# Kernel tuning notes

Measured on AMD Instinct MI355X. Metric: run time of the kernel, lower is better.

Reference implementation:

```python
import jax, jax.numpy as jnp
import numpy as np

DIM = 768
HEADS = 12
DHEAD = 64
N = 197  # 1 cls token + 14*14 patches
P = 196
KMAX = 9  # max neighborhood size (interior patch: 3x3 window)
SCALE = DHEAD ** -0.5


def _build_neighbors():
    """Reproduce the module's hard-coded kv_list; pad to KMAX with a mask."""
    top = set(range(2, 14))
    down = set(range(184, 196))
    left = set(range(15, 170, 14))
    right = set(range(28, 183, 14))
    idx = np.zeros((P, KMAX), np.int32)
    msk = np.zeros((P, KMAX), np.float32)
    for i in range(1, 197):
        if i == 1:
            nb = [1, 2, 15, 16]
        elif i == 14:
            nb = [13, 14, 27, 28]
        elif i == 183:
            nb = [169, 170, 183, 184]
        elif i == 196:
            nb = [181, 182, 195, 196]
        elif i in top:
            nb = [i - 1, i, i + 1, i + 13, i + 14, i + 15]
        elif i in left:
            nb = [i - 14, i - 13, i, i + 1, i + 14, i + 15]
        elif i in right:
            nb = [i - 15, i - 14, i - 1, i, i + 13, i + 14]
        elif i in down:
            nb = [i - 15, i - 14, i - 13, i - 1, i, i + 1]
        else:
            nb = [i - 15, i - 14, i - 13, i - 1, i, i + 1, i + 13, i + 14, i + 15]
        L = len(nb)
        idx[i - 1, :L] = nb
        msk[i - 1, :L] = 1.0
    return jnp.asarray(idx), jnp.asarray(msk)

NBR_IDX, NBR_MASK = _build_neighbors()


def setup_inputs() -> dict:
    key = jax.random.key(0)
    ks = jax.random.split(key, 10)
    b = 128
    w = lambda k: jax.random.normal(k, (DIM, DIM), jnp.float32) * 0.02
    bia = lambda k: jax.random.normal(k, (DIM,), jnp.float32) * 0.02
    return {
        "x_qkv": jax.random.normal(ks[0], (b, N, DIM), jnp.float32),
        "y_q": jax.random.normal(ks[1], (b, N, DIM), jnp.float32),
        "Wq": w(ks[2]), "bq": bia(ks[3]),
        "Wk": w(ks[4]), "bk": bia(ks[5]),
        "Wv": w(ks[6]), "bv": bia(ks[7]),
        "Wo": w(ks[8]), "bo": bia(ks[9]),
    }


def reference(x_qkv, y_q, Wq, bq, Wk, bk, Wv, bv, Wo, bo):
    b = x_qkv.shape[0]
    split = lambda t: t.reshape(b, N, HEADS, DHEAD).transpose(0, 2, 1, 3)  # b h n d
    k = split(x_qkv @ Wk + bk)
    v = split(x_qkv @ Wv + bv)
    q = split(y_q @ Wq + bq)

    # token 0 (cls): full attention over all N keys
    dots0 = jnp.einsum('bhd,bhjd->bhj', q[:, :, 0], k) * SCALE
    out0 = jnp.einsum('bhj,bhjd->bhd', jax.nn.softmax(dots0, axis=-1), v)[:, :, None]  # b h 1 d

    # patches 1..196: gather local windows (padded to KMAX, masked)
    kn = k[:, :, NBR_IDX]  # b h P KMAX d
    vn = v[:, :, NBR_IDX]
    dots = jnp.einsum('bhpd,bhpjd->bhpj', q[:, :, 1:], kn) * SCALE
    big_neg = jnp.asarray(jnp.finfo(dots.dtype).min, dots.dtype)
    dots = jnp.where(NBR_MASK > 0, dots, big_neg)
    attn = jax.nn.softmax(dots, axis=-1)
    outp = jnp.einsum('bhpj,bhpjd->bhpd', attn, vn)  # b h P d

    out = jnp.concatenate([out0, outp], axis=2)           # b h N d
    out = out.transpose(0, 2, 1, 3).reshape(b, N, HEADS * DHEAD)
    return out @ Wo + bo  # dropout: eval mode (identity)
```

## Files before the change

kernel.cpp:

```cpp
#include <hip/hip_runtime.h>


typedef __bf16 bf16x8 __attribute__((ext_vector_type(8)));
typedef float f32x4 __attribute__((ext_vector_type(4)));

#define NTOK 197
#define BATCH 128
#define MROWS (BATCH * NTOK)
#define MTILES_FULL (MROWS / 128)
#define NB_FULL (6 * MTILES_FULL)
#define W_ELEMS ((size_t)768 * 768)
#define BUF_ELEMS_FULL ((size_t)MROWS * 768)
#define PATCH_NBLK (BATCH * 49 * 12 / 4)

#define CHUNK_B 8
#define NCHUNK 16
#define MC_CHUNK (CHUNK_B * NTOK)
#define MTILES_CHUNK 13
#define BUF_ELEMS_CHUNK ((size_t)MC_CHUNK * 768)

__device__ __forceinline__ unsigned short f2b(float f) {
  unsigned int x = __float_as_uint(f);
  x += 0x7fff + ((x >> 16) & 1);
  return (unsigned short)(x >> 16);
}

__device__ __forceinline__ uint4 cvt8pack(float4 f0, float4 f1) {
  unsigned short t8[8] = { f2b(f0.x), f2b(f0.y), f2b(f0.z), f2b(f0.w),
                           f2b(f1.x), f2b(f1.y), f2b(f1.z), f2b(f1.w) };
  return *(const uint4*)t8;
}

#define GLOAD_LDS16(gp, lp)                                                   \
  __builtin_amdgcn_global_load_lds(                                           \
      (const __attribute__((address_space(1))) void*)(gp),                    \
      (__attribute__((address_space(3))) void*)(lp), 16, 0, 0)

__device__ __forceinline__ int xcd_swizzle(int bid, int nb) {
  const int q = nb >> 3, r = nb & 7;
  const int xcd = bid & 7, i = bid >> 3;
  return (xcd < r ? xcd * (q + 1) : r * (q + 1) + (xcd - r) * q) + i;
}

__global__ void transpose768x4(const float* __restrict__ s0, const float* __restrict__ s1,
                               const float* __restrict__ s2, const float* __restrict__ s3,
                               unsigned short* __restrict__ d0, unsigned short* __restrict__ d1,
                               unsigned short* __restrict__ d2, unsigned short* __restrict__ d3) {
  const float* src;
  unsigned short* dst;
  switch (blockIdx.y) {
    case 0: src = s0; dst = d0; break;
    case 1: src = s1; dst = d1; break;
    case 2: src = s2; dst = d2; break;
    default: src = s3; dst = d3; break;
  }
  int idx = blockIdx.x * 256 + threadIdx.x;
  int n = idx / 768, k = idx % 768;
  dst[idx] = f2b(src[k * 768 + n]);
}

__global__ void cvt8(const float* __restrict__ src, unsigned short* __restrict__ dst,
                     const int n8) {
  int i = blockIdx.x * 256 + threadIdx.x;
  if (i >= n8) return;
  const float4* p = (const float4*)(src + (size_t)i * 8);
  *(uint4*)(dst + (size_t)i * 8) = cvt8pack(p[0], p[1]);
}

__device__ __forceinline__ void mfma_tile(const unsigned short* sA, const unsigned short* sB,
                                          f32x4 (&acc)[4][4],
                                          const int wr, const int wc,
                                          const int lane16, const int quad) {
  bf16x8 af[4], bf_[4];
  #pragma unroll
  for (int i = 0; i < 4; ++i)
    af[i] = *(const bf16x8*)&sA[(wr * 64 + i * 16 + lane16) * 32 + quad * 8];
  #pragma unroll
  for (int j = 0; j < 4; ++j)
    bf_[j] = *(const bf16x8*)&sB[(wc * 64 + j * 16 + lane16) * 32 + quad * 8];
  #pragma unroll
  for (int i = 0; i < 4; ++i)
    #pragma unroll
    for (int j = 0; j < 4; ++j)
      acc[i][j] = __builtin_amdgcn_mfma_f32_16x16x32_bf16(af[i], bf_[j], acc[i][j], 0, 0, 0);
}

__device__ __forceinline__ void mfma_tile_kv(const unsigned short* sA,
                                             const unsigned short* sBk,
                                             const unsigned short* sBv,
                                             f32x4 (&aK)[4][4], f32x4 (&aV)[4][4],
                                             const int wr, const int wc,
                                             const int lane16, const int quad) {
  bf16x8 af[4], b1[4], b2[4];
  #pragma unroll
  for (int i = 0; i < 4; ++i)
    af[i] = *(const bf16x8*)&sA[(wr * 64 + i * 16 + lane16) * 32 + quad * 8];
  #pragma unroll
  for (int j = 0; j < 4; ++j) {
    b1[j] = *(const bf16x8*)&sBk[(wc * 64 + j * 16 + lane16) * 32 + quad * 8];
    b2[j] = *(const bf16x8*)&sBv[(wc * 64 + j * 16 + lane16) * 32 + quad * 8];
  }
  #pragma unroll
  for (int i = 0; i < 4; ++i)
    #pragma unroll
    for (int j = 0; j < 4; ++j) {
      aK[i][j] = __builtin_amdgcn_mfma_f32_16x16x32_bf16(af[i], b1[j], aK[i][j], 0, 0, 0);
      aV[i][j] = __builtin_amdgcn_mfma_f32_16x16x32_bf16(af[i], b2[j], aV[i][j], 0, 0, 0);
    }
}

__device__ __forceinline__ void epilogue128(f32x4 (&acc)[4][4], const float* __restrict__ bias,
                                            float* __restrict__ C, const int row0, const int n0,
                                            const int wr, const int wc,
                                            const int lane16, const int quad) {
  #pragma unroll
  for (int j = 0; j < 4; ++j) {
    const int col = n0 + wc * 64 + j * 16 + lane16;
    const float bv = bias[col];
    #pragma unroll
    for (int i = 0; i < 4; ++i) {
      const int r0 = row0 + wr * 64 + i * 16 + quad * 4;
      #pragma unroll
      for (int r = 0; r < 4; ++r)
        C[(size_t)(r0 + r) * 768 + col] = acc[i][j][r] + bv;
    }
  }
}

__global__ __launch_bounds__(256, 2) void kv_gemm(
    const unsigned short* __restrict__ Xb,
    const unsigned short* __restrict__ WkT, const unsigned short* __restrict__ WvT,
    const float* __restrict__ bk, const float* __restrict__ bv,
    float* __restrict__ K, float* __restrict__ V) {
  __shared__ unsigned short lds[2][3][4096];
  const int swz = xcd_swizzle(blockIdx.x, NB_FULL);
  const int by = swz / 6, bx = swz % 6;
  const int row0 = by * 128, n0 = bx * 128;
  const int tid = threadIdx.x;
  const int l = tid & 63, w = tid >> 6;
  const int wr = w >> 1, wc = w & 1;
  const int lane16 = l & 15, quad = l >> 4;
  const int rr = tid >> 2, c8 = (tid & 3) * 8;
  const int wbase = (tid & 192) * 8;

  const unsigned short* a0 = Xb + (size_t)(row0 + rr) * 768 + c8;
  const unsigned short* a1 = a0 + (size_t)64 * 768;
  const unsigned short* k0p = WkT + (size_t)(n0 + rr) * 768 + c8;
  const unsigned short* k1p = k0p + (size_t)64 * 768;
  const unsigned short* v0p = WvT + (size_t)(n0 + rr) * 768 + c8;
  const unsigned short* v1p = v0p + (size_t)64 * 768;

  f32x4 aK[4][4] = {}, aV[4][4] = {};

#define STAGE_KV(B, kt) do { const int ko = (kt) * 32;            \
    GLOAD_LDS16(a0 + ko, &lds[B][0][wbase]);                      \
    GLOAD_LDS16(a1 + ko, &lds[B][0][wbase + 2048]);               \
    GLOAD_LDS16(k0p + ko, &lds[B][1][wbase]);                     \
    GLOAD_LDS16(k1p + ko, &lds[B][1][wbase + 2048]);              \
    GLOAD_LDS16(v0p + ko, &lds[B][2][wbase]);                     \
    GLOAD_LDS16(v1p + ko, &lds[B][2][wbase + 2048]); } while (0)

  STAGE_KV(0, 0);
  __syncthreads();
  for (int kt = 0; kt < 23; ++kt) {
    const int cur = kt & 1;
    STAGE_KV(cur ^ 1, kt + 1);
    mfma_tile_kv(&lds[cur][0][0], &lds[cur][1][0], &lds[cur][2][0],
                 aK, aV, wr, wc, lane16, quad);
    __syncthreads();
  }
  mfma_tile_kv(&lds[1][0][0], &lds[1][1][0], &lds[1][2][0],
               aK, aV, wr, wc, lane16, quad);
#undef STAGE_KV

  epilogue128(aK, bk, K, row0, n0, wr, wc, lane16, quad);
  epilogue128(aV, bv, V, row0, n0, wr, wc, lane16, quad);
}

__global__ __launch_bounds__(256, 2) void o_gemm(
    const unsigned short* __restrict__ Ab, const unsigned short* __restrict__ WoT,
    const float* __restrict__ bo, float* __restrict__ C) {
  __shared__ unsigned short lds[2][2][4096];
  const int swz = xcd_swizzle(blockIdx.x, NB_FULL);
  const int by = swz / 6, bx = swz % 6;
  const int row0 = by * 128, n0 = bx * 128;
  const int tid = threadIdx.x;
  const int l = tid & 63, w = tid >> 6;
  const int wr = w >> 1, wc = w & 1;
  const int lane16 = l & 15, quad = l >> 4;
  const int rr = tid >> 2, c8 = (tid & 3) * 8;
  const int wbase = (tid & 192) * 8;

  const unsigned short* a0 = Ab + (size_t)(row0 + rr) * 768 + c8;
  const unsigned short* a1 = a0 + (size_t)64 * 768;
  const unsigned short* b0 = WoT + (size_t)(n0 + rr) * 768 + c8;
  const unsigned short* b1 = b0 + (size_t)64 * 768;

  f32x4 acc[4][4] = {};

#define STAGE_O(B, kt) do { const int ko = (kt) * 32;             \
    GLOAD_LDS16(a0 + ko, &lds[B][0][wbase]);                      \
    GLOAD_LDS16(a1 + ko, &lds[B][0][wbase + 2048]);               \
    GLOAD_LDS16(b0 + ko, &lds[B][1][wbase]);                      \
    GLOAD_LDS16(b1 + ko, &lds[B][1][wbase + 2048]); } while (0)

  STAGE_O(0, 0);
  __syncthreads();
  for (int kt = 0; kt < 23; ++kt) {
    const int cur = kt & 1;
    STAGE_O(cur ^ 1, kt + 1);
    mfma_tile(&lds[cur][0][0], &lds[cur][1][0], acc, wr, wc, lane16, quad);
    __syncthreads();
  }
  mfma_tile(&lds[1][0][0], &lds[1][1][0], acc, wr, wc, lane16, quad);
#undef STAGE_O

  epilogue128(acc, bo, C, row0, n0, wr, wc, lane16, quad);
}

__global__ __launch_bounds__(256, 2) void q_gemm(
    const float* __restrict__ Y, const unsigned short* __restrict__ WqT,
    const float* __restrict__ bq, float* __restrict__ Q) {
  __shared__ unsigned short As[2][4096];
  __shared__ unsigned short Bs[2][4096];
  const int swz = xcd_swizzle(blockIdx.x, NB_FULL);
  const int by = swz / 6, bx = swz % 6;
  const int row0 = by * 128, n0 = bx * 128;
  const int tid = threadIdx.x;
  const int l = tid & 63, w = tid >> 6;
  const int wr = w >> 1, wc = w & 1;
  const int lane16 = l & 15, quad = l >> 4;
  const int rr = tid >> 2, c8 = (tid & 3) * 8;
  const int wbase = (tid & 192) * 8;

  const float* y0 = Y + (size_t)(row0 + rr) * 768 + c8;
  const float* y1 = y0 + (size_t)64 * 768;
  const unsigned short* b0 = WqT + (size_t)(n0 + rr) * 768 + c8;
  const unsigned short* b1 = b0 + (size_t)64 * 768;

  f32x4 acc[4][4] = {};

  float4 f0 = *(const float4*)y0, f1 = *(const float4*)(y0 + 4);
  float4 g0 = *(const float4*)y1, g1 = *(const float4*)(y1 + 4);
  GLOAD_LDS16(b0, &Bs[0][wbase]);
  GLOAD_LDS16(b1, &Bs[0][wbase + 2048]);
  *(uint4*)&As[0][rr * 32 + c8] = cvt8pack(f0, f1);
  *(uint4*)&As[0][(64 + rr) * 32 + c8] = cvt8pack(g0, g1);
  __syncthreads();

  for (int kt = 0; kt < 23; ++kt) {
    const int cur = kt & 1, nxt = cur ^ 1;
    const int ko = (kt + 1) * 32;
    f0 = *(const float4*)(y0 + ko); f1 = *(const float4*)(y0 + ko + 4);
    g0 = *(const float4*)(y1 + ko); g1 = *(const float4*)(y1 + ko + 4);
    GLOAD_LDS16(b0 + ko, &Bs[nxt][wbase]);
    GLOAD_LDS16(b1 + ko, &Bs[nxt][wbase + 2048]);
    mfma_tile(&As[cur][0], &Bs[cur][0], acc, wr, wc, lane16, quad);
    *(uint4*)&As[nxt][rr * 32 + c8] = cvt8pack(f0, f1);
    *(uint4*)&As[nxt][(64 + rr) * 32 + c8] = cvt8pack(g0, g1);
    __syncthreads();
  }
  mfma_tile(&As[1][0], &Bs[1][0], acc, wr, wc, lane16, quad);

  epilogue128(acc, bq, Q, row0, n0, wr, wc, lane16, quad);
}

__device__ __forceinline__ void gemm_body_f32A(
    const float* __restrict__ A, const unsigned short* __restrict__ Wt,
    const float* __restrict__ bias, float* __restrict__ C,
    const int row0, const int n0, const int Mrows, unsigned short* sAB) {
  const int tid = threadIdx.x;
  const int l = tid & 63, w = tid >> 6;
  const int wr = w >> 1, wc = w & 1;
  const int lane16 = l & 15, quad = l >> 4;

  f32x4 acc[4][4] = {};

  for (int kt = 0; kt < 24; ++kt) {
    const int k0 = kt * 32;
    #pragma unroll
    for (int i = 0; i < 2; ++i) {
      const int ch = i * 256 + tid;
      const int rr2 = ch >> 2;
      const int c82 = (ch & 3) * 8;
      int ra = row0 + rr2; if (ra > Mrows - 1) ra = Mrows - 1;
      const float* ap = A + (size_t)ra * 768 + k0 + c82;
      float4 q0 = *(const float4*)ap;
      float4 q1 = *(const float4*)(ap + 4);
      *(uint4*)&sAB[rr2 * 32 + c82] = cvt8pack(q0, q1);
      uint4 vb = *(const uint4*)(Wt + (size_t)(n0 + rr2) * 768 + k0 + c82);
      *(uint4*)&sAB[4096 + rr2 * 32 + c82] = vb;
    }
    __syncthreads();
    mfma_tile(sAB, sAB + 4096, acc, wr, wc, lane16, quad);
    __syncthreads();
  }
  #pragma unroll
  for (int j = 0; j < 4; ++j) {
    const int col = n0 + wc * 64 + j * 16 + lane16;
    const float bv = bias[col];
    #pragma unroll
    for (int i = 0; i < 4; ++i) {
      const int r0 = row0 + wr * 64 + i * 16 + quad * 4;
      #pragma unroll
      for (int r = 0; r < 4; ++r)
        if (r0 + r < Mrows)
          C[(size_t)(r0 + r) * 768 + col] = acc[i][j][r] + bv;
    }
  }
}

__global__ __launch_bounds__(256, 2) void qkv_gemm(
    const float* __restrict__ X, const float* __restrict__ Y,
    const unsigned short* __restrict__ WkT, const unsigned short* __restrict__ WvT,
    const unsigned short* __restrict__ WqT,
    const float* __restrict__ bk, const float* __restrict__ bv, const float* __restrict__ bq,
    float* __restrict__ K, float* __restrict__ V, float* __restrict__ Q,
    const int Mrows) {
  __shared__ unsigned short sAB[8192];
  const int mat = blockIdx.x / 6;
  const int n0 = (blockIdx.x % 6) * 128;
  const float* A = (mat == 2) ? Y : X;
  const unsigned short* Wt = (mat == 0) ? WkT : (mat == 1) ? WvT : WqT;
  const float* bias = (mat == 0) ? bk : (mat == 1) ? bv : bq;
  float* C = (mat == 0) ? K : (mat == 1) ? V : Q;
  gemm_body_f32A(A, Wt, bias, C, blockIdx.y * 128, n0, Mrows, sAB);
}

__global__ __launch_bounds__(256, 2) void gemm_bt(
    const float* __restrict__ A, const unsigned short* __restrict__ Wt,
    const float* __restrict__ bias, float* __restrict__ C, const int Mrows) {
  __shared__ unsigned short sAB[8192];
  gemm_body_f32A(A, Wt, bias, C, blockIdx.y * 128, blockIdx.x * 128, Mrows, sAB);
}

__device__ __forceinline__ float cls_attn_body(const float* __restrict__ Q,
                                               const float* __restrict__ K,
                                               const float* __restrict__ V,
                                               const size_t rowbase,
                                               float* q, float* attn, float* red) {
  const int tid = threadIdx.x, l = tid & 63, w = tid >> 6;
  if (tid < 64) q[tid] = Q[rowbase + tid];
  __syncthreads();

  float d = -3e38f;
  if (tid < NTOK) {
    const float4* Kp = (const float4*)(K + rowbase + (size_t)tid * 768);
    float s = 0.f;
    #pragma unroll
    for (int u = 0; u < 16; ++u) {
      float4 kk = Kp[u];
      s += q[u * 4 + 0] * kk.x + q[u * 4 + 1] * kk.y
         + q[u * 4 + 2] * kk.z + q[u * 4 + 3] * kk.w;
    }
    d = s * 0.125f;
  }
  float m = d;
  #pragma unroll
  for (int off = 32; off; off >>= 1) m = fmaxf(m, __shfl_xor(m, off, 64));
  if (l == 0) red[w] = m;
  __syncthreads();
  const float M = fmaxf(fmaxf(red[0], red[1]), fmaxf(red[2], red[3]));
  float e = (tid < NTOK) ? __expf(d - M) : 0.f;
  float ssum = e;
  #pragma unroll
  for (int off = 32; off; off >>= 1) ssum += __shfl_xor(ssum, off, 64);
  if (l == 0) red[4 + w] = ssum;
  __syncthreads();
  const float S = red[4] + red[5] + red[6] + red[7];
  attn[tid] = e / S;
  __syncthreads();
  float o = 0.f;
  if (tid < 64) {
    for (int j = 0; j < NTOK; ++j)
      o += attn[j] * V[rowbase + (size_t)j * 768 + tid];
  }
  return o;
}

__global__ void cls_attn_b(const float* __restrict__ Q, const float* __restrict__ K,
                           const float* __restrict__ V, unsigned short* __restrict__ ATT) {
  __shared__ float q[64];
  __shared__ float attn[256];
  __shared__ float red[8];
  const int b = blockIdx.x / 12, h = blockIdx.x % 12;
  const size_t rowbase = ((size_t)b * NTOK) * 768 + h * 64;
  float o = cls_attn_body(Q, K, V, rowbase, q, attn, red);
  if (threadIdx.x < 64) ATT[rowbase + threadIdx.x] = f2b(o);
}

__global__ void cls_attn(const float* __restrict__ Q, const float* __restrict__ K,
                         const float* __restrict__ V, float* __restrict__ ATT) {
  __shared__ float q[64];
  __shared__ float attn[256];
  __shared__ float red[8];
  const int b = blockIdx.x / 12, h = blockIdx.x % 12;
  const size_t rowbase = ((size_t)b * NTOK) * 768 + h * 64;
  float o = cls_attn_body(Q, K, V, rowbase, q, attn, red);
  if (threadIdx.x < 64) ATT[rowbase + threadIdx.x] = o;
}

__global__ __launch_bounds__(256) void patch_attn4_b(
    const float* __restrict__ Q, const float* __restrict__ K,
    const float* __restrict__ V, unsigned short* __restrict__ ATT) {
  const int swb = xcd_swizzle(blockIdx.x, PATCH_NBLK);
  const int wu = swb * 4 + (threadIdx.x >> 6);
  const int l = threadIdx.x & 63;
  const int t16 = l & 15, pg = l >> 4;
  const int h = wu % 12;
  const int t2 = wu / 12;
  const int pq = t2 % 49;
  const int b = t2 / 49;
  const int p = pq * 4 + pg;
  const int r = p / 14, c = p % 14;
  const size_t ib = ((size_t)b * NTOK) * 768 + h * 64 + t16 * 4;

  const float4 q = *(const float4*)(Q + ib + (size_t)(p + 1) * 768);

  float s[9];
  int tok[9];
  #pragma unroll
  for (int jj = 0; jj < 9; ++jj) {
    const int nr = r + jj / 3 - 1, nc = c + jj % 3 - 1;
    const bool ok = ((unsigned)nr < 14u) && ((unsigned)nc < 14u);
    tok[jj] = ok ? (1 + nr * 14 + nc) : (p + 1);
    const float4 kk = *(const float4*)(K + ib + (size_t)tok[jj] * 768);
    float d = q.x * kk.x + q.y * kk.y + q.z * kk.z + q.w * kk.w;
    d += __shfl_xor(d, 1);
    d += __shfl_xor(d, 2);
    d += __shfl_xor(d, 4);
    d += __shfl_xor(d, 8);
    s[jj] = ok ? d * 0.125f : -3e38f;
  }
  float m = s[0];
  #pragma unroll
  for (int jj = 1; jj < 9; ++jj) m = fmaxf(m, s[jj]);
  float sum = 0.f;
  #pragma unroll
  for (int jj = 0; jj < 9; ++jj) { s[jj] = __expf(s[jj] - m); sum += s[jj]; }
  const float inv = 1.f / sum;

  float4 o = {0.f, 0.f, 0.f, 0.f};
  #pragma unroll
  for (int jj = 0; jj < 9; ++jj) {
    const float4 vv = *(const float4*)(V + ib + (size_t)tok[jj] * 768);
    o.x += s[jj] * vv.x; o.y += s[jj] * vv.y;
    o.z += s[jj] * vv.z; o.w += s[jj] * vv.w;
  }
  o.x *= inv; o.y *= inv; o.z *= inv; o.w *= inv;
  unsigned short t4[4] = { f2b(o.x), f2b(o.y), f2b(o.z), f2b(o.w) };
  *(ushort2*)&ATT[ib + (size_t)(p + 1) * 768] = *(const ushort2*)&t4[0];
  *(ushort2*)&ATT[ib + (size_t)(p + 1) * 768 + 2] = *(const ushort2*)&t4[2];
}

__device__ __forceinline__ float patch_attn_body(const float* __restrict__ Q,
                                                 const float* __restrict__ K,
                                                 const float* __restrict__ V,
                                                 const size_t base, const int p,
                                                 const int r, const int c) {
  const float qd = Q[base + (size_t)(p + 1) * 768];

  float s[9];
  int tok[9];
  #pragma unroll
  for (int jj = 0; jj < 9; ++jj) {
    const int nr = r + jj / 3 - 1, nc = c + jj % 3 - 1;
    const bool ok = ((unsigned)nr < 14u) && ((unsigned)nc < 14u);
    tok[jj] = ok ? (1 + nr * 14 + nc) : (p + 1);
    float d = qd * K[base + (size_t)tok[jj] * 768];
    #pragma unroll
    for (int off = 32; off; off >>= 1) d += __shfl_xor(d, off, 64);
    s[jj] = ok ? d * 0.125f : -3e38f;
  }
  float m = s[0];
  #pragma unroll
  for (int jj = 1; jj < 9; ++jj) m = fmaxf(m, s[jj]);
  float sum = 0.f;
  #pragma unroll
  for (int jj = 0; jj < 9; ++jj) { s[jj] = __expf(s[jj] - m); sum += s[jj]; }
  const float inv = 1.f / sum;
  float o = 0.f;
  #pragma unroll
  for (int jj = 0; jj < 9; ++jj) o += s[jj] * V[base + (size_t)tok[jj] * 768];
  return o * inv;
}

__global__ void patch_attn(const float* __restrict__ Q, const float* __restrict__ K,
                           const float* __restrict__ V, float* __restrict__ ATT) {
  const int wgid = blockIdx.x * 4 + (threadIdx.x >> 6);
  const int l = threadIdx.x & 63;
  const int h = wgid % 12;
  const int t2 = wgid / 12;
  const int p = t2 % 196;
  const int b = t2 / 196;
  const int r = p / 14, c = p % 14;
  const size_t base = ((size_t)b * NTOK) * 768 + h * 64 + l;
  float o = patch_attn_body(Q, K, V, base, p, r, c);
  ATT[base + (size_t)(p + 1) * 768] = o;
}

extern "C" void kernel_launch(void* const* d_in, const int* in_sizes, int n_in,
                              void* d_out, int out_size, void* d_ws, size_t ws_size,
                              hipStream_t stream) {
  const float* x  = (const float*)d_in[0];
  const float* y  = (const float*)d_in[1];
  const float* Wq = (const float*)d_in[2];
  const float* bq = (const float*)d_in[3];
  const float* Wk = (const float*)d_in[4];
  const float* bk = (const float*)d_in[5];
  const float* Wv = (const float*)d_in[6];
  const float* bv = (const float*)d_in[7];
  const float* Wo = (const float*)d_in[8];
  const float* bo = (const float*)d_in[9];
  float* out = (float*)d_out;

  unsigned short* WqT = (unsigned short*)d_ws;
  unsigned short* WkT = WqT + W_ELEMS;
  unsigned short* WvT = WkT + W_ELEMS;
  unsigned short* WoT = WvT + W_ELEMS;

  transpose768x4<<<dim3(2304, 4), 256, 0, stream>>>(Wq, Wk, Wv, Wo, WqT, WkT, WvT, WoT);

  const size_t need_full = 4 * W_ELEMS * sizeof(unsigned short)
                         + BUF_ELEMS_FULL * sizeof(unsigned short)
                         + 3 * BUF_ELEMS_FULL * sizeof(float);
  if (ws_size >= need_full) {
    unsigned short* Xb = WoT + W_ELEMS;
    unsigned short* ATTb = Xb;
    float* Kc = (float*)(Xb + BUF_ELEMS_FULL);
    float* Vc = Kc + BUF_ELEMS_FULL;
    float* Qc = Vc + BUF_ELEMS_FULL;

    const int n8 = (int)(BUF_ELEMS_FULL / 8);
    cvt8<<<n8 / 256, 256, 0, stream>>>(x, Xb, n8);

    kv_gemm<<<NB_FULL, 256, 0, stream>>>(Xb, WkT, WvT, bk, bv, Kc, Vc);
    q_gemm<<<NB_FULL, 256, 0, stream>>>(y, WqT, bq, Qc);
    cls_attn_b<<<BATCH * 12, 256, 0, stream>>>(Qc, Kc, Vc, ATTb);
    patch_attn4_b<<<PATCH_NBLK, 256, 0, stream>>>(Qc, Kc, Vc, ATTb);
    o_gemm<<<NB_FULL, 256, 0, stream>>>(ATTb, WoT, bo, out);
  } else {
    float* Kc = (float*)(WoT + W_ELEMS);
    float* Vc = Kc + BUF_ELEMS_CHUNK;
    float* Qc = Vc + BUF_ELEMS_CHUNK;

    for (int c = 0; c < NCHUNK; ++c) {
      const float* xc = x + (size_t)c * BUF_ELEMS_CHUNK;
      const float* yc = y + (size_t)c * BUF_ELEMS_CHUNK;
      qkv_gemm<<<dim3(18, MTILES_CHUNK), 256, 0, stream>>>(
          xc, yc, WkT, WvT, WqT, bk, bv, bq, Kc, Vc, Qc, MC_CHUNK);
      cls_attn<<<CHUNK_B * 12, 256, 0, stream>>>(Qc, Kc, Vc, Qc);
      patch_attn<<<(CHUNK_B * 196 * 12) / 4, 256, 0, stream>>>(Qc, Kc, Vc, Qc);
      gemm_bt<<<dim3(6, MTILES_CHUNK), 256, 0, stream>>>(Qc, WoT, bo,
                                                         out + (size_t)c * BUF_ELEMS_CHUNK, MC_CHUNK);
    }
  }
}
```

Baseline: 556.1 us.

## Unify projections into one bf16 GEMM with finer pipeline sync and parallel CLS reduction

Replaces the fused K/V GEMM and the fp32-input Q GEMM with a single bf16 GEMM kernel launched four times. Y is pre-converted to bf16 with cvt8 into the reused buffer. The GEMM loop swaps __syncthreads for explicit vmcnt waits plus raw barriers, and launch bounds rise to 4 blocks per CU to allow more occupancy. CLS attention now splits the V reduction across all four waves instead of one. The cost is reading X twice and an extra conversion pass over Y.

```diff
diff --git a/kernel.cpp b/kernel.cpp
--- a/kernel.cpp
+++ b/kernel.cpp
@@ -85,30 +85,6 @@
       acc[i][j] = __builtin_amdgcn_mfma_f32_16x16x32_bf16(af[i], bf_[j], acc[i][j], 0, 0, 0);
 }
 
-__device__ __forceinline__ void mfma_tile_kv(const unsigned short* sA,
-                                             const unsigned short* sBk,
-                                             const unsigned short* sBv,
-                                             f32x4 (&aK)[4][4], f32x4 (&aV)[4][4],
-                                             const int wr, const int wc,
-                                             const int lane16, const int quad) {
-  bf16x8 af[4], b1[4], b2[4];
-  #pragma unroll
-  for (int i = 0; i < 4; ++i)
-    af[i] = *(const bf16x8*)&sA[(wr * 64 + i * 16 + lane16) * 32 + quad * 8];
-  #pragma unroll
-  for (int j = 0; j < 4; ++j) {
-    b1[j] = *(const bf16x8*)&sBk[(wc * 64 + j * 16 + lane16) * 32 + quad * 8];
-    b2[j] = *(const bf16x8*)&sBv[(wc * 64 + j * 16 + lane16) * 32 + quad * 8];
-  }
-  #pragma unroll
-  for (int i = 0; i < 4; ++i)
-    #pragma unroll
-    for (int j = 0; j < 4; ++j) {
-      aK[i][j] = __builtin_amdgcn_mfma_f32_16x16x32_bf16(af[i], b1[j], aK[i][j], 0, 0, 0);
-      aV[i][j] = __builtin_amdgcn_mfma_f32_16x16x32_bf16(af[i], b2[j], aV[i][j], 0, 0, 0);
-    }
-}
-
 __device__ __forceinline__ void epilogue128(f32x4 (&acc)[4][4], const float* __restrict__ bias,
                                             float* __restrict__ C, const int row0, const int n0,
                                             const int wr, const int wc,
@@ -127,59 +103,9 @@
   }
 }
 
-__global__ __launch_bounds__(256, 2) void kv_gemm(
-    const unsigned short* __restrict__ Xb,
-    const unsigned short* __restrict__ WkT, const unsigned short* __restrict__ WvT,
-    const float* __restrict__ bk, const float* __restrict__ bv,
-    float* __restrict__ K, float* __restrict__ V) {
-  __shared__ unsigned short lds[2][3][4096];
-  const int swz = xcd_swizzle(blockIdx.x, NB_FULL);
-  const int by = swz / 6, bx = swz % 6;
-  const int row0 = by * 128, n0 = bx * 128;
-  const int tid = threadIdx.x;
-  const int l = tid & 63, w = tid >> 6;
-  const int wr = w >> 1, wc = w & 1;
-  const int lane16 = l & 15, quad = l >> 4;
-  const int rr = tid >> 2, c8 = (tid & 3) * 8;
-  const int wbase = (tid & 192) * 8;
-
-  const unsigned short* a0 = Xb + (size_t)(row0 + rr) * 768 + c8;
-  const unsigned short* a1 = a0 + (size_t)64 * 768;
-  const unsigned short* k0p = WkT + (size_t)(n0 + rr) * 768 + c8;
-  const unsigned short* k1p = k0p + (size_t)64 * 768;
-  const unsigned short* v0p = WvT + (size_t)(n0 + rr) * 768 + c8;
-  const unsigned short* v1p = v0p + (size_t)64 * 768;
-
-  f32x4 aK[4][4] = {}, aV[4][4] = {};
-
-#define STAGE_KV(B, kt) do { const int ko = (kt) * 32;            \
-    GLOAD_LDS16(a0 + ko, &lds[B][0][wbase]);                      \
-    GLOAD_LDS16(a1 + ko, &lds[B][0][wbase + 2048]);               \
-    GLOAD_LDS16(k0p + ko, &lds[B][1][wbase]);                     \
-    GLOAD_LDS16(k1p + ko, &lds[B][1][wbase + 2048]);              \
-    GLOAD_LDS16(v0p + ko, &lds[B][2][wbase]);                     \
-    GLOAD_LDS16(v1p + ko, &lds[B][2][wbase + 2048]); } while (0)
-
-  STAGE_KV(0, 0);
-  __syncthreads();
-  for (int kt = 0; kt < 23; ++kt) {
-    const int cur = kt & 1;
-    STAGE_KV(cur ^ 1, kt + 1);
-    mfma_tile_kv(&lds[cur][0][0], &lds[cur][1][0], &lds[cur][2][0],
-                 aK, aV, wr, wc, lane16, quad);
-    __syncthreads();
-  }
-  mfma_tile_kv(&lds[1][0][0], &lds[1][1][0], &lds[1][2][0],
-               aK, aV, wr, wc, lane16, quad);
-#undef STAGE_KV
-
-  epilogue128(aK, bk, K, row0, n0, wr, wc, lane16, quad);
-  epilogue128(aV, bv, V, row0, n0, wr, wc, lane16, quad);
-}
-
-__global__ __launch_bounds__(256, 2) void o_gemm(
-    const unsigned short* __restrict__ Ab, const unsigned short* __restrict__ WoT,
-    const float* __restrict__ bo, float* __restrict__ C) {
+__global__ __launch_bounds__(256, 4) void gemm_bf16(
+    const unsigned short* __restrict__ A, const unsigned short* __restrict__ Bt,
+    const float* __restrict__ bias, float* __restrict__ C) {
   __shared__ unsigned short lds[2][2][4096];
   const int swz = xcd_swizzle(blockIdx.x, NB_FULL);
   const int by = swz / 6, bx = swz % 6;
@@ -191,78 +117,37 @@
   const int rr = tid >> 2, c8 = (tid & 3) * 8;
   const int wbase = (tid & 192) * 8;
 
-  const unsigned short* a0 = Ab + (size_t)(row0 + rr) * 768 + c8;
+  const unsigned short* a0 = A + (size_t)(row0 + rr) * 768 + c8;
   const unsigned short* a1 = a0 + (size_t)64 * 768;
-  const unsigned short* b0 = WoT + (size_t)(n0 + rr) * 768 + c8;
+  const unsigned short* b0 = Bt + (size_t)(n0 + rr) * 768 + c8;
   const unsigned short* b1 = b0 + (size_t)64 * 768;
 
   f32x4 acc[4][4] = {};
 
-#define STAGE_O(B, kt) do { const int ko = (kt) * 32;             \
+#define STAGE_G(B, kt) do { const int ko = (kt) * 32;             \
     GLOAD_LDS16(a0 + ko, &lds[B][0][wbase]);                      \
     GLOAD_LDS16(a1 + ko, &lds[B][0][wbase + 2048]);               \
     GLOAD_LDS16(b0 + ko, &lds[B][1][wbase]);                      \
     GLOAD_LDS16(b1 + ko, &lds[B][1][wbase + 2048]); } while (0)
 
-  STAGE_O(0, 0);
-  __syncthreads();
+  STAGE_G(0, 0);
+  int cur = 0;
   for (int kt = 0; kt < 23; ++kt) {
-    const int cur = kt & 1;
-    STAGE_O(cur ^ 1, kt + 1);
+    STAGE_G(cur ^ 1, kt + 1);
+    asm volatile("s_waitcnt vmcnt(4)" ::: "memory");
+    __builtin_amdgcn_s_barrier();
+    __builtin_amdgcn_sched_barrier(0);
     mfma_tile(&lds[cur][0][0], &lds[cur][1][0], acc, wr, wc, lane16, quad);
-    __syncthreads();
-  }
-  mfma_tile(&lds[1][0][0], &lds[1][1][0], acc, wr, wc, lane16, quad);
-#undef STAGE_O
-
-  epilogue128(acc, bo, C, row0, n0, wr, wc, lane16, quad);
-}
-
-__global__ __launch_bounds__(256, 2) void q_gemm(
-    const float* __restrict__ Y, const unsigned short* __restrict__ WqT,
-    const float* __restrict__ bq, float* __restrict__ Q) {
-  __shared__ unsigned short As[2][4096];
-  __shared__ unsigned short Bs[2][4096];
-  const int swz = xcd_swizzle(blockIdx.x, NB_FULL);
-  const int by = swz / 6, bx = swz % 6;
-  const int row0 = by * 128, n0 = bx * 128;
-  const int tid = threadIdx.x;
-  const int l = tid & 63, w = tid >> 6;
-  const int wr = w >> 1, wc = w & 1;
-  const int lane16 = l & 15, quad = l >> 4;
-  const int rr = tid >> 2, c8 = (tid & 3) * 8;
-  const int wbase = (tid & 192) * 8;
-
-  const float* y0 = Y + (size_t)(row0 + rr) * 768 + c8;
-  const float* y1 = y0 + (size_t)64 * 768;
-  const unsigned short* b0 = WqT + (size_t)(n0 + rr) * 768 + c8;
-  const unsigned short* b1 = b0 + (size_t)64 * 768;
-
-  f32x4 acc[4][4] = {};
-
-  float4 f0 = *(const float4*)y0, f1 = *(const float4*)(y0 + 4);
-  float4 g0 = *(const float4*)y1, g1 = *(const float4*)(y1 + 4);
-  GLOAD_LDS16(b0, &Bs[0][wbase]);
-  GLOAD_LDS16(b1, &Bs[0][wbase + 2048]);
-  *(uint4*)&As[0][rr * 32 + c8] = cvt8pack(f0, f1);
-  *(uint4*)&As[0][(64 + rr) * 32 + c8] = cvt8pack(g0, g1);
-  __syncthreads();
-
-  for (int kt = 0; kt < 23; ++kt) {
-    const int cur = kt & 1, nxt = cur ^ 1;
-    const int ko = (kt + 1) * 32;
-    f0 = *(const float4*)(y0 + ko); f1 = *(const float4*)(y0 + ko + 4);
-    g0 = *(const float4*)(y1 + ko); g1 = *(const float4*)(y1 + ko + 4);
-    GLOAD_LDS16(b0 + ko, &Bs[nxt][wbase]);
-    GLOAD_LDS16(b1 + ko, &Bs[nxt][wbase + 2048]);
-    mfma_tile(&As[cur][0], &Bs[cur][0], acc, wr, wc, lane16, quad);
-    *(uint4*)&As[nxt][rr * 32 + c8] = cvt8pack(f0, f1);
-    *(uint4*)&As[nxt][(64 + rr) * 32 + c8] = cvt8pack(g0, g1);
-    __syncthreads();
-  }
-  mfma_tile(&As[1][0], &Bs[1][0], acc, wr, wc, lane16, quad);
-
-  epilogue128(acc, bq, Q, row0, n0, wr, wc, lane16, quad);
+    __builtin_amdgcn_s_barrier();
+    cur ^= 1;
+  }
+  asm volatile("s_waitcnt vmcnt(0)" ::: "memory");
+  __builtin_amdgcn_s_barrier();
+  __builtin_amdgcn_sched_barrier(0);
+  mfma_tile(&lds[cur][0][0], &lds[cur][1][0], acc, wr, wc, lane16, quad);
+#undef STAGE_G
+
+  epilogue128(acc, bias, C, row0, n0, wr, wc, lane16, quad);
 }
 
 __device__ __forceinline__ void gemm_body_f32A(
@@ -334,6 +219,59 @@
   gemm_body_f32A(A, Wt, bias, C, blockIdx.y * 128, blockIdx.x * 128, Mrows, sAB);
 }
 
+__global__ void cls_attn_b(const float* __restrict__ Q, const float* __restrict__ K,
+                           const float* __restrict__ V, unsigned short* __restrict__ ATT) {
+  __shared__ float q[64];
+  __shared__ float attn[256];
+  __shared__ float red[8];
+  __shared__ float part[4][64];
+  const int tid = threadIdx.x, l = tid & 63, w = tid >> 6;
+  const int b = blockIdx.x / 12, h = blockIdx.x % 12;
+  const size_t rowbase = ((size_t)b * NTOK) * 768 + h * 64;
+
+  if (tid < 64) q[tid] = Q[rowbase + tid];
+  __syncthreads();
+
+  float d = -3e38f;
+  if (tid < NTOK) {
+    const float4* Kp = (const float4*)(K + rowbase + (size_t)tid * 768);
+    float s = 0.f;
+    #pragma unroll
+    for (int u = 0; u < 16; ++u) {
+      float4 kk = Kp[u];
+      s += q[u * 4 + 0] * kk.x + q[u * 4 + 1] * kk.y
+         + q[u * 4 + 2] * kk.z + q[u * 4 + 3] * kk.w;
+    }
+    d = s * 0.125f;
+  }
+  float m = d;
+  #pragma unroll
+  for (int off = 32; off; off >>= 1) m = fmaxf(m, __shfl_xor(m, off, 64));
+  if (l == 0) red[w] = m;
+  __syncthreads();
+  const float M = fmaxf(fmaxf(red[0], red[1]), fmaxf(red[2], red[3]));
+  float e = (tid < NTOK) ? __expf(d - M) : 0.f;
+  float ssum = e;
+  #pragma unroll
+  for (int off = 32; off; off >>= 1) ssum += __shfl_xor(ssum, off, 64);
+  if (l == 0) red[4 + w] = ssum;
+  __syncthreads();
+  const float S = red[4] + red[5] + red[6] + red[7];
+  attn[tid] = e / S;
+  __syncthreads();
+
+  const int dd = tid & 63, jg = tid >> 6;
+  float o = 0.f;
+  for (int j = jg; j < NTOK; j += 4)
+    o += attn[j] * V[rowbase + (size_t)j * 768 + dd];
+  part[jg][dd] = o;
+  __syncthreads();
+  if (tid < 64) {
+    const float r = part[0][tid] + part[1][tid] + part[2][tid] + part[3][tid];
+    ATT[rowbase + tid] = f2b(r);
+  }
+}
+
 __device__ __forceinline__ float cls_attn_body(const float* __restrict__ Q,
                                                const float* __restrict__ K,
                                                const float* __restrict__ V,
@@ -376,17 +314,6 @@
       o += attn[j] * V[rowbase + (size_t)j * 768 + tid];
   }
   return o;
-}
-
-__global__ void cls_attn_b(const float* __restrict__ Q, const float* __restrict__ K,
-                           const float* __restrict__ V, unsigned short* __restrict__ ATT) {
-  __shared__ float q[64];
-  __shared__ float attn[256];
-  __shared__ float red[8];
-  const int b = blockIdx.x / 12, h = blockIdx.x % 12;
-  const size_t rowbase = ((size_t)b * NTOK) * 768 + h * 64;
-  float o = cls_attn_body(Q, K, V, rowbase, q, attn, red);
-  if (threadIdx.x < 64) ATT[rowbase + threadIdx.x] = f2b(o);
 }
 
 __global__ void cls_attn(const float* __restrict__ Q, const float* __restrict__ K,
@@ -525,20 +452,20 @@
                          + BUF_ELEMS_FULL * sizeof(unsigned short)
                          + 3 * BUF_ELEMS_FULL * sizeof(float);
   if (ws_size >= need_full) {
-    unsigned short* Xb = WoT + W_ELEMS;
-    unsigned short* ATTb = Xb;
-    float* Kc = (float*)(Xb + BUF_ELEMS_FULL);
+    unsigned short* R1 = WoT + W_ELEMS;
+    float* Kc = (float*)(R1 + BUF_ELEMS_FULL);
     float* Vc = Kc + BUF_ELEMS_FULL;
     float* Qc = Vc + BUF_ELEMS_FULL;
 
     const int n8 = (int)(BUF_ELEMS_FULL / 8);
-    cvt8<<<n8 / 256, 256, 0, stream>>>(x, Xb, n8);
-
-    kv_gemm<<<NB_FULL, 256, 0, stream>>>(Xb, WkT, WvT, bk, bv, Kc, Vc);
-    q_gemm<<<NB_FULL, 256, 0, stream>>>(y, WqT, bq, Qc);
-    cls_attn_b<<<BATCH * 12, 256, 0, stream>>>(Qc, Kc, Vc, ATTb);
-    patch_attn4_b<<<PATCH_NBLK, 256, 0, stream>>>(Qc, Kc, Vc, ATTb);
-    o_gemm<<<NB_FULL, 256, 0, stream>>>(ATTb, WoT, bo, out);
+    cvt8<<<n8 / 256, 256, 0, stream>>>(x, R1, n8);
+    gemm_bf16<<<NB_FULL, 256, 0, stream>>>(R1, WkT, bk, Kc);
+    gemm_bf16<<<NB_FULL, 256, 0, stream>>>(R1, WvT, bv, Vc);
+    cvt8<<<n8 / 256, 256, 0, stream>>>(y, R1, n8);
+    gemm_bf16<<<NB_FULL, 256, 0, stream>>>(R1, WqT, bq, Qc);
+    cls_attn_b<<<BATCH * 12, 256, 0, stream>>>(Qc, Kc, Vc, R1);
+    patch_attn4_b<<<PATCH_NBLK, 256, 0, stream>>>(Qc, Kc, Vc, R1);
+    gemm_bf16<<<NB_FULL, 256, 0, stream>>>(R1, WoT, bo, out);
   } else {
     float* Kc = (float*)(WoT + W_ELEMS);
     float* Vc = Kc + BUF_ELEMS_CHUNK;
```

Result: faster. 511.9 us (-8.0%).
